# Kernel tuning notes

Measured on AMD Instinct MI355X. Metric: run time of the kernel, lower is better.

Reference implementation:

```python
import jax, jax.numpy as jnp
import numpy as np

B, V, F, O = 256, 512, 256, 2


def setup_inputs() -> dict:
    key = jax.random.key(0)
    k1, k2, k3, k4, k5, k6 = jax.random.split(key, 6)
    features = jax.random.normal(k1, (B, V, F), dtype=jnp.float32)
    graphs = jax.random.randint(k2, (B, V, V), 0, 2, dtype=jnp.int32)
    # GCNConv params: lin (no bias) weight [F, O] + separate bias [O]
    conv_weight = jax.random.normal(k3, (F, O), dtype=jnp.float32) / np.sqrt(F)
    conv_bias = jax.random.normal(k4, (O,), dtype=jnp.float32) * 0.01
    # head: Linear(O*V, 1)
    lin_weight = jax.random.normal(k5, (1, O * V), dtype=jnp.float32) / np.sqrt(O * V)
    lin_bias = jax.random.normal(k6, (1,), dtype=jnp.float32) * 0.01
    return {"features": features, "graphs": graphs, "conv_weight": conv_weight,
            "conv_bias": conv_bias, "lin_weight": lin_weight, "lin_bias": lin_bias}


def reference(features, graphs, conv_weight, conv_bias, lin_weight, lin_bias):
    # dense_to_sparse -> binary edges (edge values discarded, weight 1)
    adj = (graphs != 0).astype(features.dtype)  # [B, V, V]
    # gcn_norm: add remaining self-loops (diag = 1), symmetric normalization
    eye = jnp.eye(V, dtype=features.dtype)
    adj = jnp.where(eye > 0, 1.0, adj)
    deg = adj.sum(axis=-1)  # [B, V]
    dinv = jnp.where(deg > 0, jax.lax.rsqrt(jnp.maximum(deg, 1e-30)), 0.0)
    norm_adj = dinv[:, :, None] * adj * dinv[:, None, :]  # D^-1/2 (A+I) D^-1/2
    # GCNConv: aggregate then affine (order commutes): A_hat X W + b
    h = jnp.einsum("bvw,bwf,fo->bvo", norm_adj, features, conv_weight) + conv_bias
    h = jax.nn.relu(h).reshape(B, V * O)  # flatten(start_dim=1) of [B, V, O]
    logits = h @ lin_weight.T + lin_bias  # [B, 1]
    return jax.nn.sigmoid(logits)
```

## Files before the change

### kernel.cpp

```cpp
#include <hip/hip_runtime.h>

#define Bn 256
#define Vn 512
#define Fn 256

#define WS_PACKED_OFF 0
#define WS_DINV_OFF   8388608
#define WS_Y_OFF      8912896

__global__ __launch_bounds__(256) void pack_deg_kernel(
    const int* __restrict__ G,
    unsigned long long* __restrict__ P,
    float* __restrict__ dinv) {
  int gid  = blockIdx.x * 256 + threadIdx.x;
  int row  = gid >> 6;
  int lane = gid & 63;
  int v    = row & (Vn - 1);

  const int* r = G + (size_t)row * Vn;
  int x0 = r[  0 + lane];
  int x1 = r[ 64 + lane];
  int x2 = r[128 + lane];
  int x3 = r[192 + lane];
  int x4 = r[256 + lane];
  int x5 = r[320 + lane];
  int x6 = r[384 + lane];
  int x7 = r[448 + lane];

  unsigned long long m0 = __ballot(x0 != 0);
  unsigned long long m1 = __ballot(x1 != 0);
  unsigned long long m2 = __ballot(x2 != 0);
  unsigned long long m3 = __ballot(x3 != 0);
  unsigned long long m4 = __ballot(x4 != 0);
  unsigned long long m5 = __ballot(x5 != 0);
  unsigned long long m6 = __ballot(x6 != 0);
  unsigned long long m7 = __ballot(x7 != 0);

  int j = v >> 6;
  unsigned long long db = 1ull << (v & 63);
  if (j == 0) m0 |= db;
  else if (j == 1) m1 |= db;
  else if (j == 2) m2 |= db;
  else if (j == 3) m3 |= db;
  else if (j == 4) m4 |= db;
  else if (j == 5) m5 |= db;
  else if (j == 6) m6 |= db;
  else             m7 |= db;

  int deg = __popcll(m0) + __popcll(m1) + __popcll(m2) + __popcll(m3) +
            __popcll(m4) + __popcll(m5) + __popcll(m6) + __popcll(m7);

  unsigned long long sel = m0;
  sel = (lane == 1) ? m1 : sel;
  sel = (lane == 2) ? m2 : sel;
  sel = (lane == 3) ? m3 : sel;
  sel = (lane == 4) ? m4 : sel;
  sel = (lane == 5) ? m5 : sel;
  sel = (lane == 6) ? m6 : sel;
  sel = (lane == 7) ? m7 : sel;
  if (lane < 8) P[(size_t)row * 8 + lane] = sel;
  if (lane == 0) dinv[row] = rsqrtf((float)deg);
}

__global__ __launch_bounds__(256) void xw_kernel(
    const float* __restrict__ X,
    const float* __restrict__ W,
    float2* __restrict__ Y) {
  int gid  = blockIdx.x * 256 + threadIdx.x;
  int row  = gid >> 6;
  int lane = gid & 63;

  const float4* xr = (const float4*)(X + (size_t)row * Fn);
  float4 x = xr[lane];
  const float4* wr = (const float4*)W;
  float4 w0 = wr[lane * 2];
  float4 w1 = wr[lane * 2 + 1];

  float s0 = x.x * w0.x + x.y * w0.z + x.z * w1.x + x.w * w1.z;
  float s1 = x.x * w0.y + x.y * w0.w + x.z * w1.y + x.w * w1.w;
  #pragma unroll
  for (int off = 32; off; off >>= 1) {
    s0 += __shfl_xor(s0, off);
    s1 += __shfl_xor(s1, off);
  }
  if (lane == 0) Y[row] = make_float2(s0, s1);
}

__global__ __launch_bounds__(256) void agg_head_kernel(
    const unsigned long long* __restrict__ P,
    const float* __restrict__ dinv,
    const float2* __restrict__ Y,
    const float* __restrict__ lw,
    const float* __restrict__ lb,
    const float* __restrict__ cb,
    float* __restrict__ out) {
  __shared__ float2 ylds[Vn];
  __shared__ float wsum[4];

  int b = blockIdx.x;
  int t = threadIdx.x;

  #pragma unroll
  for (int i = t; i < Vn; i += 256) {
    float  d = dinv[b * Vn + i];
    float2 y = Y[b * Vn + i];
    ylds[i] = make_float2(y.x * d, y.y * d);
  }
  __syncthreads();

  int v0 = t, v1 = t + 256;
  const unsigned long long* p0 = P + ((size_t)b * Vn + v0) * 8;
  const unsigned long long* p1 = P + ((size_t)b * Vn + v1) * 8;

  float a00 = 0.f, a01 = 0.f, a10 = 0.f, a11 = 0.f;
  for (int j = 0; j < 8; ++j) {
    unsigned long long m0 = p0[j];
    unsigned long long m1 = p1[j];
    const float2* yj = ylds + j * 64;
    #pragma unroll
    for (int k = 0; k < 64; ++k) {
      float2 y = yj[k];
      float s0 = (float)((m0 >> k) & 1ull);
      float s1 = (float)((m1 >> k) & 1ull);
      a00 = fmaf(s0, y.x, a00);
      a01 = fmaf(s0, y.y, a01);
      a10 = fmaf(s1, y.x, a10);
      a11 = fmaf(s1, y.y, a11);
    }
  }

  float d0 = dinv[b * Vn + v0];
  float d1 = dinv[b * Vn + v1];
  float cb0 = cb[0], cb1 = cb[1];
  const float2* lw2 = (const float2*)lw;
  float2 w0v = lw2[v0];
  float2 w1v = lw2[v1];

  float h00 = fmaxf(fmaf(d0, a00, cb0), 0.f);
  float h01 = fmaxf(fmaf(d0, a01, cb1), 0.f);
  float h10 = fmaxf(fmaf(d1, a10, cb0), 0.f);
  float h11 = fmaxf(fmaf(d1, a11, cb1), 0.f);
  float c = h00 * w0v.x + h01 * w0v.y + h10 * w1v.x + h11 * w1v.y;

  #pragma unroll
  for (int off = 32; off; off >>= 1) c += __shfl_xor(c, off);
  if ((t & 63) == 0) wsum[t >> 6] = c;
  __syncthreads();
  if (t == 0) {
    float logit = wsum[0] + wsum[1] + wsum[2] + wsum[3] + lb[0];
    out[b] = 1.0f / (1.0f + expf(-logit));
  }
}

extern "C" void kernel_launch(void* const* d_in, const int* in_sizes, int n_in,
                              void* d_out, int out_size, void* d_ws, size_t ws_size,
                              hipStream_t stream) {
  const float* features = (const float*)d_in[0];
  const int*   graphs   = (const int*)d_in[1];
  const float* conv_w   = (const float*)d_in[2];
  const float* conv_b   = (const float*)d_in[3];
  const float* lin_w    = (const float*)d_in[4];
  const float* lin_b    = (const float*)d_in[5];
  float* out = (float*)d_out;

  char* ws = (char*)d_ws;
  unsigned long long* P = (unsigned long long*)(ws + WS_PACKED_OFF);
  float*  dinv = (float*)(ws + WS_DINV_OFF);
  float2* Y    = (float2*)(ws + WS_Y_OFF);

  pack_deg_kernel<<<dim3(32768), dim3(256), 0, stream>>>(graphs, P, dinv);
  xw_kernel<<<dim3(32768), dim3(256), 0, stream>>>(features, conv_w, Y);
  agg_head_kernel<<<dim3(Bn), dim3(256), 0, stream>>>(P, dinv, Y, lin_w, lin_b, conv_b, out);
}
```

Measured before the change: 450.2 us.

## Fuse adjacency packing with XW projection and widen aggregation blocks

Merges the adjacency bit-packing/degree kernel and the feature-times-weight kernel into one launch, so each wave reads a graph row and a feature row together. Graph rows are now loaded as int4, which changes the bit layout of the packed masks to an interleaved order, and the aggregation kernel indexes LDS to match. The aggregation kernel moves to 512 threads per batch with one vertex per thread, giving more parallelism per block. The cost is more registers per thread in the fused kernel and a more intricate mask-to-vertex mapping that must stay consistent across both kernels.

```diff
diff --git a/kernel.cpp b/kernel.cpp
--- a/kernel.cpp
+++ b/kernel.cpp
@@ -8,47 +8,58 @@
 #define WS_DINV_OFF   8388608
 #define WS_Y_OFF      8912896
 
-__global__ __launch_bounds__(256) void pack_deg_kernel(
+__global__ __launch_bounds__(256) void fused_pack_xw_kernel(
     const int* __restrict__ G,
+    const float* __restrict__ X,
+    const float* __restrict__ W,
     unsigned long long* __restrict__ P,
-    float* __restrict__ dinv) {
+    float* __restrict__ dinv,
+    float2* __restrict__ Y) {
   int gid  = blockIdx.x * 256 + threadIdx.x;
   int row  = gid >> 6;
   int lane = gid & 63;
   int v    = row & (Vn - 1);
 
-  const int* r = G + (size_t)row * Vn;
-  int x0 = r[  0 + lane];
-  int x1 = r[ 64 + lane];
-  int x2 = r[128 + lane];
-  int x3 = r[192 + lane];
-  int x4 = r[256 + lane];
-  int x5 = r[320 + lane];
-  int x6 = r[384 + lane];
-  int x7 = r[448 + lane];
+  const int4* g4 = (const int4*)(G + (size_t)row * Vn);
+  int4 A0 = g4[lane];
+  int4 A1 = g4[64 + lane];
 
-  unsigned long long m0 = __ballot(x0 != 0);
-  unsigned long long m1 = __ballot(x1 != 0);
-  unsigned long long m2 = __ballot(x2 != 0);
-  unsigned long long m3 = __ballot(x3 != 0);
-  unsigned long long m4 = __ballot(x4 != 0);
-  unsigned long long m5 = __ballot(x5 != 0);
-  unsigned long long m6 = __ballot(x6 != 0);
-  unsigned long long m7 = __ballot(x7 != 0);
+  const float4* xr = (const float4*)(X + (size_t)row * Fn);
+  float4 x = xr[lane];
+  const float4* wr = (const float4*)W;
+  float4 w0 = wr[lane * 2];
+  float4 w1 = wr[lane * 2 + 1];
 
-  int j = v >> 6;
-  unsigned long long db = 1ull << (v & 63);
-  if (j == 0) m0 |= db;
-  else if (j == 1) m1 |= db;
-  else if (j == 2) m2 |= db;
-  else if (j == 3) m3 |= db;
-  else if (j == 4) m4 |= db;
-  else if (j == 5) m5 |= db;
-  else if (j == 6) m6 |= db;
-  else             m7 |= db;
+  unsigned long long m0 = __ballot(A0.x != 0);
+  unsigned long long m1 = __ballot(A0.y != 0);
+  unsigned long long m2 = __ballot(A0.z != 0);
+  unsigned long long m3 = __ballot(A0.w != 0);
+  unsigned long long m4 = __ballot(A1.x != 0);
+  unsigned long long m5 = __ballot(A1.y != 0);
+  unsigned long long m6 = __ballot(A1.z != 0);
+  unsigned long long m7 = __ballot(A1.w != 0);
+
+  int widx = ((v >> 8) << 2) | (v & 3);
+  unsigned long long db = 1ull << ((v >> 2) & 63);
+  if      (widx == 0) m0 |= db;
+  else if (widx == 1) m1 |= db;
+  else if (widx == 2) m2 |= db;
+  else if (widx == 3) m3 |= db;
+  else if (widx == 4) m4 |= db;
+  else if (widx == 5) m5 |= db;
+  else if (widx == 6) m6 |= db;
+  else                m7 |= db;
 
   int deg = __popcll(m0) + __popcll(m1) + __popcll(m2) + __popcll(m3) +
             __popcll(m4) + __popcll(m5) + __popcll(m6) + __popcll(m7);
+
+  float s0 = x.x * w0.x + x.y * w0.z + x.z * w1.x + x.w * w1.z;
+  float s1 = x.x * w0.y + x.y * w0.w + x.z * w1.y + x.w * w1.w;
+  #pragma unroll
+  for (int off = 32; off; off >>= 1) {
+    s0 += __shfl_xor(s0, off);
+    s1 += __shfl_xor(s1, off);
+  }
 
   unsigned long long sel = m0;
   sel = (lane == 1) ? m1 : sel;
@@ -59,34 +70,13 @@
   sel = (lane == 6) ? m6 : sel;
   sel = (lane == 7) ? m7 : sel;
   if (lane < 8) P[(size_t)row * 8 + lane] = sel;
-  if (lane == 0) dinv[row] = rsqrtf((float)deg);
+  if (lane == 0) {
+    dinv[row] = rsqrtf((float)deg);
+    Y[row] = make_float2(s0, s1);
+  }
 }
 
-__global__ __launch_bounds__(256) void xw_kernel(
-    const float* __restrict__ X,
-    const float* __restrict__ W,
-    float2* __restrict__ Y) {
-  int gid  = blockIdx.x * 256 + threadIdx.x;
-  int row  = gid >> 6;
-  int lane = gid & 63;
-
-  const float4* xr = (const float4*)(X + (size_t)row * Fn);
-  float4 x = xr[lane];
-  const float4* wr = (const float4*)W;
-  float4 w0 = wr[lane * 2];
-  float4 w1 = wr[lane * 2 + 1];
-
-  float s0 = x.x * w0.x + x.y * w0.z + x.z * w1.x + x.w * w1.z;
-  float s1 = x.x * w0.y + x.y * w0.w + x.z * w1.y + x.w * w1.w;
-  #pragma unroll
-  for (int off = 32; off; off >>= 1) {
-    s0 += __shfl_xor(s0, off);
-    s1 += __shfl_xor(s1, off);
-  }
-  if (lane == 0) Y[row] = make_float2(s0, s1);
-}
-
-__global__ __launch_bounds__(256) void agg_head_kernel(
+__global__ __launch_bounds__(512) void agg_head_kernel(
     const unsigned long long* __restrict__ P,
     const float* __restrict__ dinv,
     const float2* __restrict__ Y,
@@ -95,59 +85,63 @@
     const float* __restrict__ cb,
     float* __restrict__ out) {
   __shared__ float2 ylds[Vn];
-  __shared__ float wsum[4];
+  __shared__ float wsum[8];
 
   int b = blockIdx.x;
   int t = threadIdx.x;
 
-  #pragma unroll
-  for (int i = t; i < Vn; i += 256) {
-    float  d = dinv[b * Vn + i];
-    float2 y = Y[b * Vn + i];
-    ylds[i] = make_float2(y.x * d, y.y * d);
+  float d;
+  {
+    d = dinv[b * Vn + t];
+    float2 y = Y[b * Vn + t];
+    ylds[t] = make_float2(y.x * d, y.y * d);
   }
   __syncthreads();
 
-  int v0 = t, v1 = t + 256;
-  const unsigned long long* p0 = P + ((size_t)b * Vn + v0) * 8;
-  const unsigned long long* p1 = P + ((size_t)b * Vn + v1) * 8;
+  const ulonglong2* p2 = (const ulonglong2*)(P + ((size_t)b * Vn + t) * 8);
 
-  float a00 = 0.f, a01 = 0.f, a10 = 0.f, a11 = 0.f;
-  for (int j = 0; j < 8; ++j) {
-    unsigned long long m0 = p0[j];
-    unsigned long long m1 = p1[j];
-    const float2* yj = ylds + j * 64;
+  float a0 = 0.f, a1 = 0.f;
+  for (int jj = 0; jj < 4; ++jj) {
+    ulonglong2 mm = p2[jj];
     #pragma unroll
-    for (int k = 0; k < 64; ++k) {
-      float2 y = yj[k];
-      float s0 = (float)((m0 >> k) & 1ull);
-      float s1 = (float)((m1 >> k) & 1ull);
-      a00 = fmaf(s0, y.x, a00);
-      a01 = fmaf(s0, y.y, a01);
-      a10 = fmaf(s1, y.x, a10);
-      a11 = fmaf(s1, y.y, a11);
+    for (int h = 0; h < 2; ++h) {
+      unsigned long long m = h ? mm.y : mm.x;
+      int j = jj * 2 + h;
+      const float2* base = ylds + ((j >> 2) << 8) + (j & 3);
+      unsigned lo = (unsigned)m;
+      unsigned hi = (unsigned)(m >> 32);
+      #pragma unroll
+      for (int k = 0; k < 32; ++k) {
+        float s = (float)((lo >> k) & 1u);
+        float2 y = base[4 * k];
+        a0 = fmaf(s, y.x, a0);
+        a1 = fmaf(s, y.y, a1);
+      }
+      #pragma unroll
+      for (int k = 0; k < 32; ++k) {
+        float s = (float)((hi >> k) & 1u);
+        float2 y = base[4 * k + 128];
+        a0 = fmaf(s, y.x, a0);
+        a1 = fmaf(s, y.y, a1);
+      }
     }
   }
 
-  float d0 = dinv[b * Vn + v0];
-  float d1 = dinv[b * Vn + v1];
   float cb0 = cb[0], cb1 = cb[1];
   const float2* lw2 = (const float2*)lw;
-  float2 w0v = lw2[v0];
-  float2 w1v = lw2[v1];
+  float2 wv = lw2[t];
 
-  float h00 = fmaxf(fmaf(d0, a00, cb0), 0.f);
-  float h01 = fmaxf(fmaf(d0, a01, cb1), 0.f);
-  float h10 = fmaxf(fmaf(d1, a10, cb0), 0.f);
-  float h11 = fmaxf(fmaf(d1, a11, cb1), 0.f);
-  float c = h00 * w0v.x + h01 * w0v.y + h10 * w1v.x + h11 * w1v.y;
+  float h0 = fmaxf(fmaf(d, a0, cb0), 0.f);
+  float h1 = fmaxf(fmaf(d, a1, cb1), 0.f);
+  float c = h0 * wv.x + h1 * wv.y;
 
   #pragma unroll
   for (int off = 32; off; off >>= 1) c += __shfl_xor(c, off);
   if ((t & 63) == 0) wsum[t >> 6] = c;
   __syncthreads();
   if (t == 0) {
-    float logit = wsum[0] + wsum[1] + wsum[2] + wsum[3] + lb[0];
+    float logit = wsum[0] + wsum[1] + wsum[2] + wsum[3] +
+                  wsum[4] + wsum[5] + wsum[6] + wsum[7] + lb[0];
     out[b] = 1.0f / (1.0f + expf(-logit));
   }
 }
@@ -168,7 +162,8 @@
   float*  dinv = (float*)(ws + WS_DINV_OFF);
   float2* Y    = (float2*)(ws + WS_Y_OFF);
 
-  pack_deg_kernel<<<dim3(32768), dim3(256), 0, stream>>>(graphs, P, dinv);
-  xw_kernel<<<dim3(32768), dim3(256), 0, stream>>>(features, conv_w, Y);
-  agg_head_kernel<<<dim3(Bn), dim3(256), 0, stream>>>(P, dinv, Y, lin_w, lin_b, conv_b, out);
+  fused_pack_xw_kernel<<<dim3(32768), dim3(256), 0, stream>>>(
+      graphs, features, conv_w, P, dinv, Y);
+  agg_head_kernel<<<dim3(Bn), dim3(512), 0, stream>>>(
+      P, dinv, Y, lin_w, lin_b, conv_b, out);
 }
```

New measurement: 442.1 us. About the same (-1.8%).
